# Optimization experiments

Measured on AMD Instinct MI355X. Metric: run time of the kernel, lower is better.

Reference implementation:

```python
import jax, jax.numpy as jnp
import numpy as np

N_CLASSES = 9
N_GROUPS = 2


def setup_inputs() -> dict:
    key = jax.random.key(0)
    k1, k2 = jax.random.split(key)
    N = 16_777_216  # number of samples
    preds = jax.random.randint(k1, (N,), 0, N_CLASSES, dtype=jnp.int32)
    attrs = jax.random.randint(k2, (N,), 0, N_GROUPS, dtype=jnp.int32)
    return {"preds": preds, "attrs": attrs}


def reference(preds, attrs):
    # Fused histogram: flatten (class, group) -> single bin id in [0, 18)
    flat = preds * N_GROUPS + attrs  # [N]
    counts = jax.ops.segment_sum(
        jnp.ones_like(flat, dtype=jnp.float32), flat,
        num_segments=N_CLASSES * N_GROUPS,
    ).reshape(N_CLASSES, N_GROUPS)  # [9, 2] histogram

    n_attr_1 = jnp.sum(attrs != 0).astype(jnp.float32)
    n_attr_0 = jnp.float32(attrs.shape[0]) - n_attr_1

    diff = counts[:, 0] / n_attr_0 - counts[:, 1] / n_attr_1  # [9]
    return jnp.sum(diff * diff)
```

## Files before the change

### kernel.cpp

```cpp
#include <hip/hip_runtime.h>


#define N_CLASSES 9
#define N_GROUPS 2
#define NBINS (N_CLASSES * N_GROUPS)
#define GRID_BLOCKS 2048

__global__ __launch_bounds__(256) void spd_hist_kernel(
    const int* __restrict__ preds,
    const int* __restrict__ attrs,
    unsigned int* __restrict__ g_counts,
    int n4, int n)
{
    __shared__ unsigned int lhist[N_CLASSES];
    if (threadIdx.x < N_CLASSES) lhist[threadIdx.x] = 0u;
    __syncthreads();

    unsigned long long acc0 = 0ull, acc1 = 0ull;

    const int4* __restrict__ p4 = (const int4*)preds;
    const int4* __restrict__ a4 = (const int4*)attrs;
    const int stride = gridDim.x * blockDim.x;

    for (int i = blockIdx.x * blockDim.x + threadIdx.x; i < n4; i += stride) {
        int4 p = p4[i];
        int4 a = a4[i];
        {
            unsigned long long inc = 1ull << (7 * p.x);
            acc0 += (a.x == 0) ? inc : 0ull;
            acc1 += (a.x == 0) ? 0ull : inc;
        }
        {
            unsigned long long inc = 1ull << (7 * p.y);
            acc0 += (a.y == 0) ? inc : 0ull;
            acc1 += (a.y == 0) ? 0ull : inc;
        }
        {
            unsigned long long inc = 1ull << (7 * p.z);
            acc0 += (a.z == 0) ? inc : 0ull;
            acc1 += (a.z == 0) ? 0ull : inc;
        }
        {
            unsigned long long inc = 1ull << (7 * p.w);
            acc0 += (a.w == 0) ? inc : 0ull;
            acc1 += (a.w == 0) ? 0ull : inc;
        }
    }

    if (blockIdx.x == 0) {
        for (int i = n4 * 4 + (int)threadIdx.x; i < n; i += (int)blockDim.x) {
            unsigned long long inc = 1ull << (7 * preds[i]);
            if (attrs[i] == 0) acc0 += inc; else acc1 += inc;
        }
    }

    unsigned int cnt[N_CLASSES];
    #pragma unroll
    for (int p = 0; p < N_CLASSES; ++p) {
        unsigned int c0 = (unsigned int)(acc0 >> (7 * p)) & 127u;
        unsigned int c1 = (unsigned int)(acc1 >> (7 * p)) & 127u;
        cnt[p] = c0 | (c1 << 16);
    }

    #pragma unroll
    for (int m = 1; m < 64; m <<= 1) {
        #pragma unroll
        for (int p = 0; p < N_CLASSES; ++p)
            cnt[p] += __shfl_xor(cnt[p], m, 64);
    }

    if ((threadIdx.x & 63) == 0) {
        #pragma unroll
        for (int p = 0; p < N_CLASSES; ++p)
            atomicAdd(&lhist[p], cnt[p]);
    }
    __syncthreads();

    if (threadIdx.x < NBINS) {
        unsigned int pk = lhist[threadIdx.x >> 1];
        unsigned int v = (threadIdx.x & 1) ? (pk >> 16) : (pk & 0xFFFFu);
        atomicAdd(&g_counts[threadIdx.x], v);
    }
}

__global__ void spd_finalize_kernel(const unsigned int* __restrict__ g_counts,
                                    float* __restrict__ out, double n_total)
{
    if (threadIdx.x == 0 && blockIdx.x == 0) {
        double n1 = 0.0;
        #pragma unroll
        for (int c = 0; c < N_CLASSES; ++c)
            n1 += (double)g_counts[c * N_GROUPS + 1];
        double n0 = n_total - n1;
        double acc = 0.0;
        #pragma unroll
        for (int c = 0; c < N_CLASSES; ++c) {
            double d = (double)g_counts[c * N_GROUPS] / n0
                     - (double)g_counts[c * N_GROUPS + 1] / n1;
            acc += d * d;
        }
        out[0] = (float)acc;
    }
}

extern "C" void kernel_launch(void* const* d_in, const int* in_sizes, int n_in,
                              void* d_out, int out_size, void* d_ws, size_t ws_size,
                              hipStream_t stream)
{
    const int* preds = (const int*)d_in[0];
    const int* attrs = (const int*)d_in[1];
    const int n = in_sizes[0];

    unsigned int* counts = (unsigned int*)d_ws;
    hipMemsetAsync(counts, 0, NBINS * sizeof(unsigned int), stream);

    const int n4 = n / 4;
    const int block = 256;
    int grid = (n4 + block - 1) / block;
    if (grid > GRID_BLOCKS) grid = GRID_BLOCKS;
    if (grid < 1) grid = 1;

    spd_hist_kernel<<<grid, block, 0, stream>>>(preds, attrs, counts, n4, n);
    spd_finalize_kernel<<<1, 64, 0, stream>>>(counts, (float*)d_out, (double)n);
}
```

Measured before the change: 158.8 us.

## Replace global atomics and memset with per-block partials reduced in finalize

Each block now writes its 18 bin counts to its own slot in the workspace instead of atomically adding into a shared global histogram. That removes the memset launch and the contended global atomics. The finalize kernel now runs 1024 threads and reduces the partials with wave shuffles. The packed 7-bit accumulators are flushed every 31 iterations, and the block histogram is split into two 32-bit arrays, so counts cannot overflow at larger N. The cost is a few extra shifts and masks in the hot loop and a larger finalize step.

```diff
diff --git a/kernel.cpp b/kernel.cpp
--- a/kernel.cpp
+++ b/kernel.cpp
@@ -5,61 +5,66 @@
 #define N_GROUPS 2
 #define NBINS (N_CLASSES * N_GROUPS)
 #define GRID_BLOCKS 2048
+#define CHUNK 31
 
 __global__ __launch_bounds__(256) void spd_hist_kernel(
     const int* __restrict__ preds,
     const int* __restrict__ attrs,
-    unsigned int* __restrict__ g_counts,
+    unsigned int* __restrict__ partials,
     int n4, int n)
 {
-    __shared__ unsigned int lhist[N_CLASSES];
-    if (threadIdx.x < N_CLASSES) lhist[threadIdx.x] = 0u;
+    __shared__ unsigned int lh0[N_CLASSES];
+    __shared__ unsigned int lh1[N_CLASSES];
+    if (threadIdx.x < N_CLASSES) { lh0[threadIdx.x] = 0u; lh1[threadIdx.x] = 0u; }
     __syncthreads();
 
-    unsigned long long acc0 = 0ull, acc1 = 0ull;
+    unsigned int cnt[N_CLASSES];
+    #pragma unroll
+    for (int p = 0; p < N_CLASSES; ++p) cnt[p] = 0u;
 
     const int4* __restrict__ p4 = (const int4*)preds;
     const int4* __restrict__ a4 = (const int4*)attrs;
     const int stride = gridDim.x * blockDim.x;
 
-    for (int i = blockIdx.x * blockDim.x + threadIdx.x; i < n4; i += stride) {
-        int4 p = p4[i];
-        int4 a = a4[i];
-        {
-            unsigned long long inc = 1ull << (7 * p.x);
-            acc0 += (a.x == 0) ? inc : 0ull;
-            acc1 += (a.x == 0) ? 0ull : inc;
+    int i = blockIdx.x * blockDim.x + threadIdx.x;
+    while (i < n4) {
+        unsigned long long acc0 = 0ull, acc1 = 0ull;
+        int lim = CHUNK;
+        for (; i < n4 && lim; i += stride, --lim) {
+            int4 p = p4[i];
+            int4 a = a4[i];
+            {
+                unsigned long long inc = 1ull << (7 * p.x);
+                acc0 += (a.x == 0) ? inc : 0ull;
+                acc1 += (a.x == 0) ? 0ull : inc;
+            }
+            {
+                unsigned long long inc = 1ull << (7 * p.y);
+                acc0 += (a.y == 0) ? inc : 0ull;
+                acc1 += (a.y == 0) ? 0ull : inc;
+            }
+            {
+                unsigned long long inc = 1ull << (7 * p.z);
+                acc0 += (a.z == 0) ? inc : 0ull;
+                acc1 += (a.z == 0) ? 0ull : inc;
+            }
+            {
+                unsigned long long inc = 1ull << (7 * p.w);
+                acc0 += (a.w == 0) ? inc : 0ull;
+                acc1 += (a.w == 0) ? 0ull : inc;
+            }
         }
-        {
-            unsigned long long inc = 1ull << (7 * p.y);
-            acc0 += (a.y == 0) ? inc : 0ull;
-            acc1 += (a.y == 0) ? 0ull : inc;
-        }
-        {
-            unsigned long long inc = 1ull << (7 * p.z);
-            acc0 += (a.z == 0) ? inc : 0ull;
-            acc1 += (a.z == 0) ? 0ull : inc;
-        }
-        {
-            unsigned long long inc = 1ull << (7 * p.w);
-            acc0 += (a.w == 0) ? inc : 0ull;
-            acc1 += (a.w == 0) ? 0ull : inc;
+        #pragma unroll
+        for (int p = 0; p < N_CLASSES; ++p) {
+            unsigned int c0 = (unsigned int)(acc0 >> (7 * p)) & 127u;
+            unsigned int c1 = (unsigned int)(acc1 >> (7 * p)) & 127u;
+            cnt[p] += c0 | (c1 << 16);
         }
     }
 
     if (blockIdx.x == 0) {
-        for (int i = n4 * 4 + (int)threadIdx.x; i < n; i += (int)blockDim.x) {
-            unsigned long long inc = 1ull << (7 * preds[i]);
-            if (attrs[i] == 0) acc0 += inc; else acc1 += inc;
-        }
-    }
-
-    unsigned int cnt[N_CLASSES];
-    #pragma unroll
-    for (int p = 0; p < N_CLASSES; ++p) {
-        unsigned int c0 = (unsigned int)(acc0 >> (7 * p)) & 127u;
-        unsigned int c1 = (unsigned int)(acc1 >> (7 * p)) & 127u;
-        cnt[p] = c0 | (c1 << 16);
+        for (int t = n4 * 4 + (int)threadIdx.x; t < n; t += (int)blockDim.x)
+            cnt[preds[t]] += (attrs[t] == 0) ? 1u : 0x10000u;
     }
 
     #pragma unroll
@@ -71,32 +76,50 @@
 
     if ((threadIdx.x & 63) == 0) {
         #pragma unroll
-        for (int p = 0; p < N_CLASSES; ++p)
-            atomicAdd(&lhist[p], cnt[p]);
+        for (int p = 0; p < N_CLASSES; ++p) {
+            atomicAdd(&lh0[p], cnt[p] & 0xFFFFu);
+            atomicAdd(&lh1[p], cnt[p] >> 16);
+        }
     }
     __syncthreads();
 
     if (threadIdx.x < NBINS) {
-        unsigned int pk = lhist[threadIdx.x >> 1];
-        unsigned int v = (threadIdx.x & 1) ? (pk >> 16) : (pk & 0xFFFFu);
-        atomicAdd(&g_counts[threadIdx.x], v);
+        int c = threadIdx.x >> 1;
+        unsigned int v = (threadIdx.x & 1) ? lh1[c] : lh0[c];
+        partials[blockIdx.x * NBINS + threadIdx.x] = v;
     }
 }
 
-__global__ void spd_finalize_kernel(const unsigned int* __restrict__ g_counts,
-                                    float* __restrict__ out, double n_total)
+__global__ __launch_bounds__(1024) void spd_finalize_kernel(
+    const unsigned int* __restrict__ partials,
+    float* __restrict__ out, int nblocks, double n_total)
 {
-    if (threadIdx.x == 0 && blockIdx.x == 0) {
+    __shared__ double counts[NBINS];
+    const int tid = threadIdx.x;
+
+    if (tid < NBINS * 32) {
+        const int bin = tid >> 5;
+        const int j = tid & 31;
+        unsigned int s = 0u;
+        for (int b = j; b < nblocks; b += 32)
+            s += partials[b * NBINS + bin];
+        #pragma unroll
+        for (int m = 1; m < 32; m <<= 1)
+            s += __shfl_xor(s, m, 32);
+        if (j == 0) counts[bin] = (double)s;
+    }
+    __syncthreads();
+
+    if (tid == 0) {
         double n1 = 0.0;
         #pragma unroll
         for (int c = 0; c < N_CLASSES; ++c)
-            n1 += (double)g_counts[c * N_GROUPS + 1];
+            n1 += counts[c * N_GROUPS + 1];
         double n0 = n_total - n1;
         double acc = 0.0;
         #pragma unroll
         for (int c = 0; c < N_CLASSES; ++c) {
-            double d = (double)g_counts[c * N_GROUPS] / n0
-                     - (double)g_counts[c * N_GROUPS + 1] / n1;
+            double d = counts[c * N_GROUPS] / n0 - counts[c * N_GROUPS + 1] / n1;
             acc += d * d;
         }
         out[0] = (float)acc;
@@ -111,15 +134,16 @@
     const int* attrs = (const int*)d_in[1];
     const int n = in_sizes[0];
 
-    unsigned int* counts = (unsigned int*)d_ws;
-    hipMemsetAsync(counts, 0, NBINS * sizeof(unsigned int), stream);
+    unsigned int* partials = (unsigned int*)d_ws;
 
     const int n4 = n / 4;
     const int block = 256;
     int grid = (n4 + block - 1) / block;
     if (grid > GRID_BLOCKS) grid = GRID_BLOCKS;
+    int max_grid = (int)(ws_size / (NBINS * sizeof(unsigned int)));
+    if (grid > max_grid) grid = max_grid;
     if (grid < 1) grid = 1;
 
-    spd_hist_kernel<<<grid, block, 0, stream>>>(preds, attrs, counts, n4, n);
-    spd_finalize_kernel<<<1, 64, 0, stream>>>(counts, (float*)d_out, (double)n);
+    spd_hist_kernel<<<grid, block, 0, stream>>>(preds, attrs, partials, n4, n);
+    spd_finalize_kernel<<<1, 1024, 0, stream>>>(partials, (float*)d_out, grid, (double)n);
 }
```

Measured after the change: 156.2 us. Within noise of the previous version (-1.6%).
